# Optimization experiments

Hardware: AMD Instinct MI355X
Metric: run time of the kernel (lower is better)

The kernel has to match this reference:

```python
import jax, jax.numpy as jnp
import numpy as np

N_FEATURES = 4096
IN_DIM = 4096
BATCH = 4096
NNZ = int(0.01 * N_FEATURES * IN_DIM)  # 167772, matches sparse_coo_init


def setup_inputs() -> dict:
    key = jax.random.key(0)
    k_in, k_vals, k_rows, k_cols, k_bias = jax.random.split(key, 5)
    inputs = jax.random.normal(k_in, (BATCH, IN_DIM), dtype=jnp.float32)
    kernel_vals = jax.random.normal(k_vals, (NNZ,), dtype=jnp.float32)
    kernel_rows = jax.random.randint(k_rows, (NNZ,), 0, N_FEATURES, dtype=jnp.int32)
    kernel_cols = jax.random.randint(k_cols, (NNZ,), 0, IN_DIM, dtype=jnp.int32)
    bias = jax.random.normal(k_bias, (N_FEATURES,), dtype=jnp.float32)
    return {
        "inputs": inputs,
        "kernel_vals": kernel_vals,
        "kernel_rows": kernel_rows,
        "kernel_cols": kernel_cols,
        "bias": bias,
    }


def reference(inputs, kernel_vals, kernel_rows, kernel_cols, bias):
    # COO sparse-dense matmul: A (n_features x in_dim, COO with duplicate-
    # index summation) @ inputs.T, then transpose and add bias:
    #   z = (A @ inputs.T).T + bias  ==  inputs @ A.T + bias
    # Densifying the small (4096x4096 = 64MB) kernel via scatter-add is the
    # memory-cheapest faithful form (avoids an nnz x batch intermediate) and
    # exactly reproduces COO semantics (duplicates sum).
    dense_kernel = jnp.zeros((N_FEATURES, IN_DIM), dtype=kernel_vals.dtype)
    dense_kernel = dense_kernel.at[kernel_rows, kernel_cols].add(kernel_vals)
    # [batch, in_dim] @ [in_dim, n_features] -> [batch, n_features]
    z = jnp.einsum('bd,fd->bf', inputs, dense_kernel) + bias
    return z
```

## Files before the change

kernel.cpp:

```cpp
#include <hip/hip_runtime.h>


#define NF 4096
#define IND 4096
#define BATCH_TOTAL 4096
#define FT 32
#define BT 512
#define NT_MAIN 512

typedef float f32x4 __attribute__((ext_vector_type(4)));
typedef float f32x2 __attribute__((ext_vector_type(2)));

__device__ __forceinline__ float bf2f(unsigned short u) {
    return __uint_as_float(((unsigned int)u) << 16);
}
__device__ __forceinline__ unsigned short f2bf(float x) {
    unsigned int h = __float_as_uint(x);
    h += 0x7fff + ((h >> 16) & 1);
    return (unsigned short)(h >> 16);
}

__global__ void hist_kernel(const int* __restrict__ rows,
                            int* __restrict__ cnt, int nnz) {
    int k = blockIdx.x * blockDim.x + threadIdx.x;
    if (k < nnz) atomicAdd(&cnt[rows[k]], 1);
}

__global__ __launch_bounds__(1024)
void scan_kernel(const int* __restrict__ cnt, int* __restrict__ rptr,
                 int* __restrict__ cursor) {
    __shared__ int ts[1024];
    const int t = threadIdx.x;
    const int base = t * 4;
    int e0 = cnt[base], e1 = cnt[base + 1], e2 = cnt[base + 2], e3 = cnt[base + 3];
    ts[t] = e0 + e1 + e2 + e3;
    __syncthreads();
    for (int off = 1; off < 1024; off <<= 1) {
        int v = (t >= off) ? ts[t - off] : 0;
        __syncthreads();
        ts[t] += v;
        __syncthreads();
    }
    int excl = (t == 0) ? 0 : ts[t - 1];
    int p0 = excl, p1 = excl + e0, p2 = p1 + e1, p3 = p2 + e2;
    rptr[base + 0] = p0;   cursor[base + 0] = p0;
    rptr[base + 1] = p1;   cursor[base + 1] = p1;
    rptr[base + 2] = p2;   cursor[base + 2] = p2;
    rptr[base + 3] = p3;   cursor[base + 3] = p3;
}

__global__ void scatter_pairs_kernel(const float* __restrict__ vals,
                                     const int* __restrict__ rows,
                                     const int* __restrict__ cols,
                                     int* __restrict__ cursor,
                                     int2* __restrict__ pairs, int nnz) {
    int k = blockIdx.x * blockDim.x + threadIdx.x;
    if (k < nnz) {
        int p = atomicAdd(&cursor[rows[k]], 1);
        pairs[p] = make_int2(cols[k], __float_as_int(vals[k]));
    }
}

__global__ __launch_bounds__(256)
void transpose_kernel(const float* __restrict__ in,
                      unsigned short* __restrict__ outT) {
    __shared__ float t[64][65];
    const int tb = blockIdx.x;
    const int d0 = (tb & 63) * 64;
    const int b0 = (tb >> 6) * 64;
    const int tx4 = threadIdx.x & 15;
    const int ty  = threadIdx.x >> 4;
#pragma unroll
    for (int p = 0; p < 4; ++p) {
        int brow = ty + p * 16;
        float4 v = *(const float4*)(in + (long)(b0 + brow) * IND + d0 + tx4 * 4);
        t[brow][tx4 * 4 + 0] = v.x;
        t[brow][tx4 * 4 + 1] = v.y;
        t[brow][tx4 * 4 + 2] = v.z;
        t[brow][tx4 * 4 + 3] = v.w;
    }
    __syncthreads();
    const int bx4 = threadIdx.x & 15;
    const int dy  = threadIdx.x >> 4;
#pragma unroll
    for (int p = 0; p < 4; ++p) {
        int drow = dy + p * 16;
        ushort4 o;
        o.x = f2bf(t[bx4 * 4 + 0][drow]);
        o.y = f2bf(t[bx4 * 4 + 1][drow]);
        o.z = f2bf(t[bx4 * 4 + 2][drow]);
        o.w = f2bf(t[bx4 * 4 + 3][drow]);
        *(ushort4*)(outT + (long)(d0 + drow) * BATCH_TOTAL + b0 + bx4 * 4) = o;
    }
}

__global__ __launch_bounds__(NT_MAIN, 8)
void spmm_axpy_kernel(const unsigned short* __restrict__ inT,
                      const int2* __restrict__ pairs,
                      const int* __restrict__ rptr,
                      const int* __restrict__ cnt,
                      const float* __restrict__ bias,
                      float* __restrict__ out) {
#pragma clang fp contract(fast)
    __shared__ unsigned short tile[FT][BT + 8];

    const int bid = blockIdx.x;
    const int per = gridDim.x >> 3;
    const int wg = (bid & 7) * per + (bid >> 3);
    const int fblk = wg & (NF / FT - 1);
    const int bt   = wg >> 7;
    const int b0 = bt * BT;
    const int fbase = fblk * FT;

    const int tid = threadIdx.x;
    const int wid = tid >> 6;
    const int lane = tid & 63;

    for (int fi = wid; fi < FT; fi += 8) {
        const int f = fbase + fi;
        const int start = __builtin_amdgcn_readfirstlane(rptr[f]);
        const int n     = __builtin_amdgcn_readfirstlane(cnt[f]);
        f32x2 a0 = {0.f, 0.f}, a1 = {0.f, 0.f}, a2 = {0.f, 0.f}, a3 = {0.f, 0.f};
        const unsigned short* gbase = inT + b0 + lane * 8;
#pragma unroll 4
        for (int k = 0; k < n; ++k) {
            int2 e = pairs[start + k];
            float v = __int_as_float(e.y);
            f32x2 vv = {v, v};
            uint4 u = *(const uint4*)(gbase + (long)e.x * BATCH_TOTAL);
            f32x2 x0 = {__uint_as_float(u.x << 16), __uint_as_float(u.x & 0xffff0000u)};
            f32x2 x1 = {__uint_as_float(u.y << 16), __uint_as_float(u.y & 0xffff0000u)};
            f32x2 x2 = {__uint_as_float(u.z << 16), __uint_as_float(u.z & 0xffff0000u)};
            f32x2 x3 = {__uint_as_float(u.w << 16), __uint_as_float(u.w & 0xffff0000u)};
            a0 += vv * x0;
            a1 += vv * x1;
            a2 += vv * x2;
            a3 += vv * x3;
        }
        ushort4 p0, p1;
        p0.x = f2bf(a0.x); p0.y = f2bf(a0.y); p0.z = f2bf(a1.x); p0.w = f2bf(a1.y);
        p1.x = f2bf(a2.x); p1.y = f2bf(a2.y); p1.z = f2bf(a3.x); p1.w = f2bf(a3.y);
        *(ushort4*)(&tile[fi][lane * 8])     = p0;
        *(ushort4*)(&tile[fi][lane * 8 + 4]) = p1;
    }
    __syncthreads();

    const int chunk = tid & 7;
    const int rbase = tid >> 3;
    float4 bv = ((const float4*)bias)[(fbase >> 2) + chunk];
#pragma unroll
    for (int p = 0; p < 8; ++p) {
        int r = rbase + p * 64;
        f32x4 o;
        o.x = bf2f(tile[chunk * 4 + 0][r]) + bv.x;
        o.y = bf2f(tile[chunk * 4 + 1][r]) + bv.y;
        o.z = bf2f(tile[chunk * 4 + 2][r]) + bv.z;
        o.w = bf2f(tile[chunk * 4 + 3][r]) + bv.w;
        __builtin_nontemporal_store(
            o, (f32x4*)(out + (long)(b0 + r) * NF + fbase + chunk * 4));
    }
}

__global__ void init_out_kernel(float* __restrict__ out,
                                const float* __restrict__ bias) {
    const int nf4 = NF / 4;
    const long total = (long)BATCH_TOTAL * nf4;
    const float4* b4 = (const float4*)bias;
    float4* o4 = (float4*)out;
    for (long i = (long)blockIdx.x * blockDim.x + threadIdx.x; i < total;
         i += (long)gridDim.x * blockDim.x)
        o4[i] = b4[i & (nf4 - 1)];
}

__global__ void scatter3_kernel(const float* __restrict__ vals,
                                const int* __restrict__ rows,
                                const int* __restrict__ cols,
                                int* __restrict__ cursor,
                                float* __restrict__ sval,
                                int* __restrict__ scol,
                                int* __restrict__ srow, int nnz) {
    int k = blockIdx.x * blockDim.x + threadIdx.x;
    if (k < nnz) {
        int r = rows[k];
        int p = atomicAdd(&cursor[r], 1);
        sval[p] = vals[k];
        scol[p] = cols[k];
        srow[p] = r;
    }
}

#define TILE_B_FB 4
__global__ __launch_bounds__(512, 4)
void spmm_csr_fb_kernel(const float* __restrict__ inputs,
                        const float* __restrict__ sval,
                        const int* __restrict__ scol,
                        const int* __restrict__ srow,
                        float* __restrict__ out, int nnz) {
    __shared__ float in_lds[TILE_B_FB][IND];
    const int tid = threadIdx.x;
    const long b0 = (long)blockIdx.x * TILE_B_FB;
    for (int i = tid; i < IND / 4; i += 512) {
#pragma unroll
        for (int j = 0; j < TILE_B_FB; ++j)
            ((float4*)in_lds[j])[i] = ((const float4*)(inputs + (b0 + j) * IND))[i];
    }
    __syncthreads();
    const int C = (nnz + 511) / 512;
    int k0 = tid * C, k1 = min(k0 + C, nnz);
    if (k0 < k1) {
        int cur = srow[k0];
        float a0 = 0.f, a1 = 0.f, a2 = 0.f, a3 = 0.f;
        for (int k = k0; k < k1; ++k) {
            int r = srow[k];
            float v = sval[k];
            int c = scol[k];
            if (r != cur) {
                atomicAdd(&out[(b0 + 0) * NF + cur], a0);
                atomicAdd(&out[(b0 + 1) * NF + cur], a1);
                atomicAdd(&out[(b0 + 2) * NF + cur], a2);
                atomicAdd(&out[(b0 + 3) * NF + cur], a3);
                a0 = a1 = a2 = a3 = 0.f;
                cur = r;
            }
            a0 += v * in_lds[0][c];
            a1 += v * in_lds[1][c];
            a2 += v * in_lds[2][c];
            a3 += v * in_lds[3][c];
        }
        atomicAdd(&out[(b0 + 0) * NF + cur], a0);
        atomicAdd(&out[(b0 + 1) * NF + cur], a1);
        atomicAdd(&out[(b0 + 2) * NF + cur], a2);
        atomicAdd(&out[(b0 + 3) * NF + cur], a3);
    }
}

extern "C" void kernel_launch(void* const* d_in, const int* in_sizes, int n_in,
                              void* d_out, int out_size, void* d_ws, size_t ws_size,
                              hipStream_t stream) {
    const float* inputs = (const float*)d_in[0];
    const float* vals   = (const float*)d_in[1];
    const int*   rows   = (const int*)d_in[2];
    const int*   cols   = (const int*)d_in[3];
    const float* bias   = (const float*)d_in[4];
    float* out = (float*)d_out;
    const int nnz = in_sizes[1];

    char* ws = (char*)d_ws;
    size_t off = 0;
    int* cnt    = (int*)(ws + off); off += (size_t)NF * 4;
    int* cursor = (int*)(ws + off); off += (size_t)NF * 4;
    int* rptr   = (int*)(ws + off); off += (size_t)NF * 4;
    size_t pairs_off = (off + 15) & ~(size_t)15;
    int2* pairs = (int2*)(ws + pairs_off);
    size_t after_pairs = (pairs_off + (size_t)nnz * 8 + 15) & ~(size_t)15;
    unsigned short* inT = (unsigned short*)(ws + after_pairs);
    size_t need_main = after_pairs + (size_t)IND * BATCH_TOTAL * 2;

    const int eb = (nnz + 255) / 256;

    if (need_main <= ws_size) {
        (void)hipMemsetAsync(cnt, 0, (size_t)NF * 4, stream);
        hist_kernel<<<eb, 256, 0, stream>>>(rows, cnt, nnz);
        scan_kernel<<<1, 1024, 0, stream>>>(cnt, rptr, cursor);
        scatter_pairs_kernel<<<eb, 256, 0, stream>>>(vals, rows, cols, cursor,
                                                     pairs, nnz);
        transpose_kernel<<<(IND / 64) * (BATCH_TOTAL / 64), 256, 0, stream>>>(
            inputs, inT);
        spmm_axpy_kernel<<<(NF / FT) * (BATCH_TOTAL / BT), NT_MAIN, 0, stream>>>(
            inT, pairs, rptr, cnt, bias, out);
    } else {
        int*   srow = (int*)(ws + pairs_off);
        int*   scol = srow + nnz;
        float* sval = (float*)(scol + nnz);
        (void)hipMemsetAsync(cnt, 0, (size_t)NF * 4, stream);
        init_out_kernel<<<2048, 256, 0, stream>>>(out, bias);
        hist_kernel<<<eb, 256, 0, stream>>>(rows, cnt, nnz);
        scan_kernel<<<1, 1024, 0, stream>>>(cnt, rptr, cursor);
        scatter3_kernel<<<eb, 256, 0, stream>>>(vals, rows, cols, cursor,
                                                sval, scol, srow, nnz);
        spmm_csr_fb_kernel<<<BATCH_TOTAL / TILE_B_FB, 512, 0, stream>>>(
            inputs, sval, scol, srow, out, nnz);
    }
}
```

Measured before the change: 137.9 us.

## Fuse transpose with histogram, bucket nonzeros by column half, halve feature tile

The transpose and the row histogram now run in one launch, which removes a kernel boundary. Nonzeros are bucketed by (column half, row) in an 8K-entry CSR, so every wave walks each row's entries for the low column half first and then the high half. This groups the gathers from the transposed input into a smaller column range and is meant to improve L2 locality. FT drops from 32 to 16, giving twice as many workgroups, each with 16 rows and two accumulator sets per wave. The costs are more per-row segments to walk and a larger scan.

```diff
diff --git a/kernel.cpp b/kernel.cpp
--- a/kernel.cpp
+++ b/kernel.cpp
@@ -4,9 +4,10 @@
 #define NF 4096
 #define IND 4096
 #define BATCH_TOTAL 4096
-#define FT 32
+#define FT 16
 #define BT 512
 #define NT_MAIN 512
+#define NTILES ((IND / 64) * (BATCH_TOTAL / 64))
 
 typedef float f32x4 __attribute__((ext_vector_type(4)));
 typedef float f32x2 __attribute__((ext_vector_type(2)));
@@ -18,6 +19,191 @@
     unsigned int h = __float_as_uint(x);
     h += 0x7fff + ((h >> 16) & 1);
     return (unsigned short)(h >> 16);
+}
+
+__global__ __launch_bounds__(256)
+void fused_transpose_hist(const float* __restrict__ in,
+                          unsigned short* __restrict__ outT,
+                          const int* __restrict__ rows,
+                          const int* __restrict__ cols,
+                          int* __restrict__ cnt2, int nnz) {
+    if (blockIdx.x < NTILES) {
+        __shared__ float t[64][65];
+        const int tb = blockIdx.x;
+        const int d0 = (tb & 63) * 64;
+        const int b0 = (tb >> 6) * 64;
+        const int tx4 = threadIdx.x & 15;
+        const int ty  = threadIdx.x >> 4;
+#pragma unroll
+        for (int p = 0; p < 4; ++p) {
+            int brow = ty + p * 16;
+            float4 v = *(const float4*)(in + (long)(b0 + brow) * IND + d0 + tx4 * 4);
+            t[brow][tx4 * 4 + 0] = v.x;
+            t[brow][tx4 * 4 + 1] = v.y;
+            t[brow][tx4 * 4 + 2] = v.z;
+            t[brow][tx4 * 4 + 3] = v.w;
+        }
+        __syncthreads();
+        const int bx4 = threadIdx.x & 15;
+        const int dy  = threadIdx.x >> 4;
+#pragma unroll
+        for (int p = 0; p < 4; ++p) {
+            int drow = dy + p * 16;
+            ushort4 o;
+            o.x = f2bf(t[bx4 * 4 + 0][drow]);
+            o.y = f2bf(t[bx4 * 4 + 1][drow]);
+            o.z = f2bf(t[bx4 * 4 + 2][drow]);
+            o.w = f2bf(t[bx4 * 4 + 3][drow]);
+            *(ushort4*)(outT + (long)(d0 + drow) * BATCH_TOTAL + b0 + bx4 * 4) = o;
+        }
+    } else {
+        int k = (blockIdx.x - NTILES) * 256 + threadIdx.x;
+        if (k < nnz) {
+            int key = ((cols[k] >> 11) << 12) | rows[k];
+            atomicAdd(&cnt2[key], 1);
+        }
+    }
+}
+
+__global__ __launch_bounds__(512)
+void scan8k_kernel(const int* __restrict__ cnt2, int* __restrict__ rptr2,
+                   int* __restrict__ cursor2) {
+    __shared__ int ts[512];
+    const int t = threadIdx.x;
+    const int base = t * 16;
+    int e[16];
+    int tot = 0;
+#pragma unroll
+    for (int i = 0; i < 16; ++i) { e[i] = cnt2[base + i]; tot += e[i]; }
+    ts[t] = tot;
+    __syncthreads();
+    for (int off = 1; off < 512; off <<= 1) {
+        int v = (t >= off) ? ts[t - off] : 0;
+        __syncthreads();
+        ts[t] += v;
+        __syncthreads();
+    }
+    int run = (t == 0) ? 0 : ts[t - 1];
+#pragma unroll
+    for (int i = 0; i < 16; ++i) {
+        rptr2[base + i] = run;
+        cursor2[base + i] = run;
+        run += e[i];
+    }
+}
+
+__global__ void scatter_pairs2_kernel(const float* __restrict__ vals,
+                                      const int* __restrict__ rows,
+                                      const int* __restrict__ cols,
+                                      int* __restrict__ cursor2,
+                                      int2* __restrict__ pairs, int nnz) {
+    int k = blockIdx.x * blockDim.x + threadIdx.x;
+    if (k < nnz) {
+        int c = cols[k];
+        int key = ((c >> 11) << 12) | rows[k];
+        int p = atomicAdd(&cursor2[key], 1);
+        pairs[p] = make_int2(c, __float_as_int(vals[k]));
+    }
+}
+
+__device__ __forceinline__ void walk_seg(const int2* __restrict__ pairs,
+                                         int start, int n,
+                                         const unsigned short* __restrict__ gbase,
+                                         f32x2& a0, f32x2& a1, f32x2& a2, f32x2& a3) {
+#pragma unroll 4
+    for (int k = 0; k < n; ++k) {
+        int2 e = pairs[start + k];
+        float v = __int_as_float(e.y);
+        f32x2 vv = {v, v};
+        uint4 u = *(const uint4*)(gbase + (long)e.x * BATCH_TOTAL);
+        f32x2 x0 = {__uint_as_float(u.x << 16), __uint_as_float(u.x & 0xffff0000u)};
+        f32x2 x1 = {__uint_as_float(u.y << 16), __uint_as_float(u.y & 0xffff0000u)};
+        f32x2 x2 = {__uint_as_float(u.z << 16), __uint_as_float(u.z & 0xffff0000u)};
+        f32x2 x3 = {__uint_as_float(u.w << 16), __uint_as_float(u.w & 0xffff0000u)};
+        a0 += vv * x0;
+        a1 += vv * x1;
+        a2 += vv * x2;
+        a3 += vv * x3;
+    }
+}
+
+__global__ __launch_bounds__(NT_MAIN, 8)
+void spmm_axpy_kernel(const unsigned short* __restrict__ inT,
+                      const int2* __restrict__ pairs,
+                      const int* __restrict__ rptr2,
+                      const int* __restrict__ cnt2,
+                      const float* __restrict__ bias,
+                      float* __restrict__ out) {
+#pragma clang fp contract(fast)
+    __shared__ unsigned short tile[FT][BT + 8];
+
+    const int bid = blockIdx.x;
+    const int per = gridDim.x >> 3;
+    const int wg = (bid & 7) * per + (bid >> 3);
+    const int fblk = wg & (NF / FT - 1);
+    const int bt   = wg >> 8;
+    const int b0 = bt * BT;
+    const int fbase = fblk * FT;
+
+    const int tid = threadIdx.x;
+    const int wid = tid >> 6;
+    const int lane = tid & 63;
+
+    const int fA = fbase + wid;
+    const int fB = fbase + 8 + wid;
+
+    f32x2 aA0 = {0.f, 0.f}, aA1 = {0.f, 0.f}, aA2 = {0.f, 0.f}, aA3 = {0.f, 0.f};
+    f32x2 aB0 = {0.f, 0.f}, aB1 = {0.f, 0.f}, aB2 = {0.f, 0.f}, aB3 = {0.f, 0.f};
+    const unsigned short* gbase = inT + b0 + lane * 8;
+
+#pragma unroll
+    for (int h = 0; h < 2; ++h) {
+        const int oA = h * NF + fA;
+        const int sA = __builtin_amdgcn_readfirstlane(rptr2[oA]);
+        const int nA = __builtin_amdgcn_readfirstlane(cnt2[oA]);
+        walk_seg(pairs, sA, nA, gbase, aA0, aA1, aA2, aA3);
+        const int oB = h * NF + fB;
+        const int sB = __builtin_amdgcn_readfirstlane(rptr2[oB]);
+        const int nB = __builtin_amdgcn_readfirstlane(cnt2[oB]);
+        walk_seg(pairs, sB, nB, gbase, aB0, aB1, aB2, aB3);
+    }
+
+    ushort4 p0, p1;
+    p0.x = f2bf(aA0.x); p0.y = f2bf(aA0.y); p0.z = f2bf(aA1.x); p0.w = f2bf(aA1.y);
+    p1.x = f2bf(aA2.x); p1.y = f2bf(aA2.y); p1.z = f2bf(aA3.x); p1.w = f2bf(aA3.y);
+    *(ushort4*)(&tile[wid][lane * 8])     = p0;
+    *(ushort4*)(&tile[wid][lane * 8 + 4]) = p1;
+    p0.x = f2bf(aB0.x); p0.y = f2bf(aB0.y); p0.z = f2bf(aB1.x); p0.w = f2bf(aB1.y);
+    p1.x = f2bf(aB2.x); p1.y = f2bf(aB2.y); p1.z = f2bf(aB3.x); p1.w = f2bf(aB3.y);
+    *(ushort4*)(&tile[wid + 8][lane * 8])     = p0;
+    *(ushort4*)(&tile[wid + 8][lane * 8 + 4]) = p1;
+    __syncthreads();
+
+    const int chunk = tid & 3;
+    const int rbase = tid >> 2;
+    float4 bv = ((const float4*)bias)[(fbase >> 2) + chunk];
+#pragma unroll
+    for (int p = 0; p < 4; ++p) {
+        int r = rbase + p * 128;
+        f32x4 o;
+        o.x = bf2f(tile[chunk * 4 + 0][r]) + bv.x;
+        o.y = bf2f(tile[chunk * 4 + 1][r]) + bv.y;
+        o.z = bf2f(tile[chunk * 4 + 2][r]) + bv.z;
+        o.w = bf2f(tile[chunk * 4 + 3][r]) + bv.w;
+        __builtin_nontemporal_store(
+            o, (f32x4*)(out + (long)(b0 + r) * NF + fbase + chunk * 4));
+    }
+}
+
+__global__ void init_out_kernel(float* __restrict__ out,
+                                const float* __restrict__ bias) {
+    const int nf4 = NF / 4;
+    const long total = (long)BATCH_TOTAL * nf4;
+    const float4* b4 = (const float4*)bias;
+    float4* o4 = (float4*)out;
+    for (long i = (long)blockIdx.x * blockDim.x + threadIdx.x; i < total;
+         i += (long)gridDim.x * blockDim.x)
+        o4[i] = b4[i & (nf4 - 1)];
 }
 
 __global__ void hist_kernel(const int* __restrict__ rows,
@@ -47,129 +233,6 @@
     rptr[base + 1] = p1;   cursor[base + 1] = p1;
     rptr[base + 2] = p2;   cursor[base + 2] = p2;
     rptr[base + 3] = p3;   cursor[base + 3] = p3;
-}
-
-__global__ void scatter_pairs_kernel(const float* __restrict__ vals,
-                                     const int* __restrict__ rows,
-                                     const int* __restrict__ cols,
-                                     int* __restrict__ cursor,
-                                     int2* __restrict__ pairs, int nnz) {
-    int k = blockIdx.x * blockDim.x + threadIdx.x;
-    if (k < nnz) {
-        int p = atomicAdd(&cursor[rows[k]], 1);
-        pairs[p] = make_int2(cols[k], __float_as_int(vals[k]));
-    }
-}
-
-__global__ __launch_bounds__(256)
-void transpose_kernel(const float* __restrict__ in,
-                      unsigned short* __restrict__ outT) {
-    __shared__ float t[64][65];
-    const int tb = blockIdx.x;
-    const int d0 = (tb & 63) * 64;
-    const int b0 = (tb >> 6) * 64;
-    const int tx4 = threadIdx.x & 15;
-    const int ty  = threadIdx.x >> 4;
-#pragma unroll
-    for (int p = 0; p < 4; ++p) {
-        int brow = ty + p * 16;
-        float4 v = *(const float4*)(in + (long)(b0 + brow) * IND + d0 + tx4 * 4);
-        t[brow][tx4 * 4 + 0] = v.x;
-        t[brow][tx4 * 4 + 1] = v.y;
-        t[brow][tx4 * 4 + 2] = v.z;
-        t[brow][tx4 * 4 + 3] = v.w;
-    }
-    __syncthreads();
-    const int bx4 = threadIdx.x & 15;
-    const int dy  = threadIdx.x >> 4;
-#pragma unroll
-    for (int p = 0; p < 4; ++p) {
-        int drow = dy + p * 16;
-        ushort4 o;
-        o.x = f2bf(t[bx4 * 4 + 0][drow]);
-        o.y = f2bf(t[bx4 * 4 + 1][drow]);
-        o.z = f2bf(t[bx4 * 4 + 2][drow]);
-        o.w = f2bf(t[bx4 * 4 + 3][drow]);
-        *(ushort4*)(outT + (long)(d0 + drow) * BATCH_TOTAL + b0 + bx4 * 4) = o;
-    }
-}
-
-__global__ __launch_bounds__(NT_MAIN, 8)
-void spmm_axpy_kernel(const unsigned short* __restrict__ inT,
-                      const int2* __restrict__ pairs,
-                      const int* __restrict__ rptr,
-                      const int* __restrict__ cnt,
-                      const float* __restrict__ bias,
-                      float* __restrict__ out) {
-#pragma clang fp contract(fast)
-    __shared__ unsigned short tile[FT][BT + 8];
-
-    const int bid = blockIdx.x;
-    const int per = gridDim.x >> 3;
-    const int wg = (bid & 7) * per + (bid >> 3);
-    const int fblk = wg & (NF / FT - 1);
-    const int bt   = wg >> 7;
-    const int b0 = bt * BT;
-    const int fbase = fblk * FT;
-
-    const int tid = threadIdx.x;
-    const int wid = tid >> 6;
-    const int lane = tid & 63;
-
-    for (int fi = wid; fi < FT; fi += 8) {
-        const int f = fbase + fi;
-        const int start = __builtin_amdgcn_readfirstlane(rptr[f]);
-        const int n     = __builtin_amdgcn_readfirstlane(cnt[f]);
-        f32x2 a0 = {0.f, 0.f}, a1 = {0.f, 0.f}, a2 = {0.f, 0.f}, a3 = {0.f, 0.f};
-        const unsigned short* gbase = inT + b0 + lane * 8;
-#pragma unroll 4
-        for (int k = 0; k < n; ++k) {
-            int2 e = pairs[start + k];
-            float v = __int_as_float(e.y);
-            f32x2 vv = {v, v};
-            uint4 u = *(const uint4*)(gbase + (long)e.x * BATCH_TOTAL);
-            f32x2 x0 = {__uint_as_float(u.x << 16), __uint_as_float(u.x & 0xffff0000u)};
-            f32x2 x1 = {__uint_as_float(u.y << 16), __uint_as_float(u.y & 0xffff0000u)};
-            f32x2 x2 = {__uint_as_float(u.z << 16), __uint_as_float(u.z & 0xffff0000u)};
-            f32x2 x3 = {__uint_as_float(u.w << 16), __uint_as_float(u.w & 0xffff0000u)};
-            a0 += vv * x0;
-            a1 += vv * x1;
-            a2 += vv * x2;
-            a3 += vv * x3;
-        }
-        ushort4 p0, p1;
-        p0.x = f2bf(a0.x); p0.y = f2bf(a0.y); p0.z = f2bf(a1.x); p0.w = f2bf(a1.y);
-        p1.x = f2bf(a2.x); p1.y = f2bf(a2.y); p1.z = f2bf(a3.x); p1.w = f2bf(a3.y);
-        *(ushort4*)(&tile[fi][lane * 8])     = p0;
-        *(ushort4*)(&tile[fi][lane * 8 + 4]) = p1;
-    }
-    __syncthreads();
-
-    const int chunk = tid & 7;
-    const int rbase = tid >> 3;
-    float4 bv = ((const float4*)bias)[(fbase >> 2) + chunk];
-#pragma unroll
-    for (int p = 0; p < 8; ++p) {
-        int r = rbase + p * 64;
-        f32x4 o;
-        o.x = bf2f(tile[chunk * 4 + 0][r]) + bv.x;
-        o.y = bf2f(tile[chunk * 4 + 1][r]) + bv.y;
-        o.z = bf2f(tile[chunk * 4 + 2][r]) + bv.z;
-        o.w = bf2f(tile[chunk * 4 + 3][r]) + bv.w;
-        __builtin_nontemporal_store(
-            o, (f32x4*)(out + (long)(b0 + r) * NF + fbase + chunk * 4));
-    }
-}
-
-__global__ void init_out_kernel(float* __restrict__ out,
-                                const float* __restrict__ bias) {
-    const int nf4 = NF / 4;
-    const long total = (long)BATCH_TOTAL * nf4;
-    const float4* b4 = (const float4*)bias;
-    float4* o4 = (float4*)out;
-    for (long i = (long)blockIdx.x * blockDim.x + threadIdx.x; i < total;
-         i += (long)gridDim.x * blockDim.x)
-        o4[i] = b4[i & (nf4 - 1)];
 }
 
 __global__ void scatter3_kernel(const float* __restrict__ vals,
@@ -247,9 +310,9 @@
 
     char* ws = (char*)d_ws;
     size_t off = 0;
-    int* cnt    = (int*)(ws + off); off += (size_t)NF * 4;
-    int* cursor = (int*)(ws + off); off += (size_t)NF * 4;
-    int* rptr   = (int*)(ws + off); off += (size_t)NF * 4;
+    int* cnt2    = (int*)(ws + off); off += (size_t)2 * NF * 4;
+    int* cursor2 = (int*)(ws + off); off += (size_t)2 * NF * 4;
+    int* rptr2   = (int*)(ws + off); off += (size_t)2 * NF * 4;
     size_t pairs_off = (off + 15) & ~(size_t)15;
     int2* pairs = (int2*)(ws + pairs_off);
     size_t after_pairs = (pairs_off + (size_t)nnz * 8 + 15) & ~(size_t)15;
@@ -259,16 +322,18 @@
     const int eb = (nnz + 255) / 256;
 
     if (need_main <= ws_size) {
-        (void)hipMemsetAsync(cnt, 0, (size_t)NF * 4, stream);
-        hist_kernel<<<eb, 256, 0, stream>>>(rows, cnt, nnz);
-        scan_kernel<<<1, 1024, 0, stream>>>(cnt, rptr, cursor);
-        scatter_pairs_kernel<<<eb, 256, 0, stream>>>(vals, rows, cols, cursor,
-                                                     pairs, nnz);
-        transpose_kernel<<<(IND / 64) * (BATCH_TOTAL / 64), 256, 0, stream>>>(
-            inputs, inT);
+        (void)hipMemsetAsync(cnt2, 0, (size_t)2 * NF * 4, stream);
+        fused_transpose_hist<<<NTILES + eb, 256, 0, stream>>>(
+            inputs, inT, rows, cols, cnt2, nnz);
+        scan8k_kernel<<<1, 512, 0, stream>>>(cnt2, rptr2, cursor2);
+        scatter_pairs2_kernel<<<eb, 256, 0, stream>>>(vals, rows, cols, cursor2,
+                                                      pairs, nnz);
         spmm_axpy_kernel<<<(NF / FT) * (BATCH_TOTAL / BT), NT_MAIN, 0, stream>>>(
-            inT, pairs, rptr, cnt, bias, out);
+            inT, pairs, rptr2, cnt2, bias, out);
     } else {
+        int* cnt    = cnt2;
+        int* cursor = cursor2;
+        int* rptr   = rptr2;
         int*   srow = (int*)(ws + pairs_off);
         int*   scol = srow + nnz;
         float* sval = (float*)(scol + nnz);
```

After: 115.5 us. 1.19x faster.
